# Kernel optimization log

Hardware: AMD Instinct MI355X
Metric: run time of the kernel (lower is better)

The kernel has to match this reference:

```python
import jax, jax.numpy as jnp
import numpy as np
from jax.scipy.special import gammaln, logsumexp

# Model dims (match init_kwargs)
N1, N2, N3 = 16, 16, 8          # n_state_list
S = N1 * N2 * N3                # tot_dim = 2048 flattened states
M = 16                          # m_dimensions
T = 16384                       # T_max


def setup_inputs() -> dict:
    key = jax.random.key(0)
    ks = jax.random.split(key, 10)
    # observed Poisson counts, shape (T, M)
    x = jax.random.randint(ks[0], (T, M), 0, 20)
    # per-factor Poisson rates: lambda_list[i] = exp(randn(N_i, M)) as in __init__
    lam1 = jnp.exp(jax.random.normal(ks[1], (N1, M), dtype=jnp.float32))
    lam2 = jnp.exp(jax.random.normal(ks[2], (N2, M), dtype=jnp.float32))
    lam3 = jnp.exp(jax.random.normal(ks[3], (N3, M), dtype=jnp.float32))
    # per-factor log transition matrices: softmax over dim 0 (A[next, prev] columns sum to 1)
    logA1 = jax.nn.log_softmax(jax.random.normal(ks[4], (N1, N1), dtype=jnp.float32), axis=0)
    logA2 = jax.nn.log_softmax(jax.random.normal(ks[5], (N2, N2), dtype=jnp.float32), axis=0)
    logA3 = jax.nn.log_softmax(jax.random.normal(ks[6], (N3, N3), dtype=jnp.float32), axis=0)
    # per-factor log state priors: log_softmax(rand(N)*10)
    logpi1 = jax.nn.log_softmax(jax.random.uniform(ks[7], (N1,), dtype=jnp.float32) * 10.0)
    logpi2 = jax.nn.log_softmax(jax.random.uniform(ks[8], (N2,), dtype=jnp.float32) * 10.0)
    logpi3 = jax.nn.log_softmax(jax.random.uniform(ks[9], (N3,), dtype=jnp.float32) * 10.0)
    return {"x": x, "lam1": lam1, "lam2": lam2, "lam3": lam3,
            "logA1": logA1, "logA2": logA2, "logA3": logA3,
            "logpi1": logpi1, "logpi2": logpi2, "logpi3": logpi3}


def reference(x, lam1, lam2, lam3, logA1, logA2, logA3, logpi1, logpi2, logpi3):
    # combine_lambdas: lam_c[s1,s2,s3,m] = lam1[s1,m] + lam2[s2,m] + lam3[s3,m]
    lam_c = (lam1[:, None, None, :] + lam2[None, :, None, :]
             + lam3[None, None, :, :]).reshape(S, M)  # (S, M)
    xf = x.astype(jnp.float32)
    # Poisson log-pmf summed over the M observation dims:
    # em[t, s] = sum_m x[t,m]*log(lam_c[s,m]) - lam_c[s,m] - lgamma(x[t,m]+1)
    em = (xf @ jnp.log(lam_c).T
          - lam_c.sum(axis=-1)[None, :]
          - gammaln(xf + 1.0).sum(axis=-1)[:, None])  # (T, S)
    # combined log transition: logA[dest_flat, prev_flat] = sum_i logA_i[d_i, p_i]
    logA = (logA1[:, None, None, :, None, None]
            + logA2[None, :, None, None, :, None]
            + logA3[None, None, :, None, None, :]).reshape(S, S)
    # combined log priors
    logpi = (logpi1[:, None, None] + logpi2[None, :, None]
             + logpi3[None, None, :]).reshape(S)
    # log-domain forward recurrence (log_alpha_calc)
    alpha0 = em[0] + logpi
    def step(prev, em_t):
        a = em_t + logsumexp(logA + prev[None, :], axis=1)
        return a, None
    alpha_last, _ = jax.lax.scan(step, alpha0, em[1:])
    # log p(x) = logsumexp over final-step alpha
    return logsumexp(alpha_last)
```

## Files before the change

### kernel.cpp

```cpp
#include <hip/hip_runtime.h>
#include <math.h>

#define TMAX 16384
#define MDIM 16
#define SD   2048
#define CLEN 16
#define WUP  16
#define CHKB 512
#define NS   (CLEN + WUP - 1)
#define EROWS 32

typedef unsigned int  uint;
typedef unsigned short ushort;
typedef __attribute__((ext_vector_type(8))) short short8;
typedef __attribute__((ext_vector_type(4))) short short4v;
typedef __attribute__((ext_vector_type(4))) float floatx4;
typedef __attribute__((ext_vector_type(2))) uint uintx2;

template<int CTRL>
__device__ __forceinline__ float fmax_dpp(float v) {
    int o = __builtin_amdgcn_update_dpp(__float_as_int(v), __float_as_int(v),
                                        CTRL, 0xf, 0xf, false);
    return fmaxf(v, __int_as_float(o));
}
__device__ __forceinline__ float waveMax64(float v) {
    v = fmax_dpp<0x111>(v);
    v = fmax_dpp<0x112>(v);
    v = fmax_dpp<0x114>(v);
    v = fmax_dpp<0x118>(v);
    v = fmax_dpp<0x142>(v);
    v = fmax_dpp<0x143>(v);
    return __int_as_float(__builtin_amdgcn_readlane(__float_as_int(v), 63));
}
__device__ __forceinline__ float waveSumF(float v) {
    #pragma unroll
    for (int o = 32; o > 0; o >>= 1) v += __shfl_xor(v, o, 64);
    return v;
}
__device__ __forceinline__ double waveSumD(double v) {
    #pragma unroll
    for (int o = 32; o > 0; o >>= 1) v += __shfl_xor(v, o, 64);
    return v;
}

__device__ __forceinline__ short f2bfs(float f) {
    uint u = __float_as_uint(f);
    return (short)((u + 0x7FFFu + ((u >> 16) & 1u)) >> 16);
}
__device__ __forceinline__ uint pkbf(float a, float b) {
    uint ua = __float_as_uint(a), ub = __float_as_uint(b);
    ua = (ua + 0x7FFFu + ((ua >> 16) & 1u)) >> 16;
    ub = (ub + 0x7FFFu + ((ub >> 16) & 1u)) & 0xFFFF0000u;
    return ua | ub;
}
__device__ __forceinline__ short4v pk4(float a, float b, float c, float d) {
    short4v r;
    r[0] = f2bfs(a); r[1] = f2bfs(b); r[2] = f2bfs(c); r[3] = f2bfs(d);
    return r;
}
__device__ __forceinline__ float bfl(uint u) { return __uint_as_float(u << 16); }
__device__ __forceinline__ float bfh(uint u) { return __uint_as_float(u & 0xFFFF0000u); }

#if __has_builtin(__builtin_amdgcn_mfma_f32_16x16x16bf16_1k)
#define MFMA16(a, b, c) __builtin_amdgcn_mfma_f32_16x16x16bf16_1k(a, b, c, 0, 0, 0)
#else
__device__ __forceinline__ floatx4 mfma16_asm(short4v a, short4v b, floatx4 c) {
    asm volatile("v_mfma_f32_16x16x16_bf16 %0, %1, %2, %0\n\t"
                 "s_nop 7\n\ts_nop 7"
                 : "+v"(c) : "v"(a), "v"(b));
    return c;
}
#define MFMA16(a, b, c) mfma16_asm(a, b, c)
#endif
#define MFMA32(a, b, c) __builtin_amdgcn_mfma_f32_16x16x32_bf16(a, b, c, 0, 0, 0)

__global__ __launch_bounds__(512, 2)
void emP_kernel(const int* __restrict__ x,
                const float* __restrict__ lam1,
                const float* __restrict__ lam2,
                const float* __restrict__ lam3,
                ushort* __restrict__ P,
                float* __restrict__ SumAuxArr,
                float* __restrict__ out) {
    __shared__ float wmx[EROWS][8];
    __shared__ float DemS[EROWS];
    __shared__ float lgtbl[32];
    __shared__ __align__(16) float xfs[EROWS * MDIM];
    __shared__ float lgred;
    const int tid = threadIdx.x, lane = tid & 63, wv = tid >> 6;
    const int q = lane >> 4, nn = lane & 15;
    const int d2 = 2 * wv + (nn >> 3);
    const int d3 = nn & 7;

    if (tid < 32) lgtbl[tid] = lgammaf((float)tid + 1.0f);
    if (tid == 0) lgred = 0.f;

    float llc[4][16], ls[4];
    #pragma unroll
    for (int j = 0; j < 4; ++j) {
        const int d1 = 4 * q + j;
        float sum = 0.f;
        #pragma unroll
        for (int m = 0; m < 16; ++m) {
            float la = lam1[d1 * 16 + m] + lam2[d2 * 16 + m] + lam3[d3 * 16 + m];
            sum += la;
            llc[j][m] = __logf(la);
        }
        ls[j] = sum;
    }

    const int t0 = blockIdx.x * EROWS;
    const int xv = x[t0 * MDIM + tid];
    xfs[tid] = (float)xv;
    __syncthreads();
    {
        double lg = (double)lgtbl[xv & 31];
        lg = waveSumD(lg);
        if (lane == 0) atomicAdd(&lgred, (float)lg);
    }

    float em[EROWS][4];
    #pragma unroll
    for (int ti = 0; ti < EROWS; ++ti) {
        float xr[16];
        *(float4*)&xr[0]  = *(const float4*)&xfs[ti * 16 + 0];
        *(float4*)&xr[4]  = *(const float4*)&xfs[ti * 16 + 4];
        *(float4*)&xr[8]  = *(const float4*)&xfs[ti * 16 + 8];
        *(float4*)&xr[12] = *(const float4*)&xfs[ti * 16 + 12];
        float vm = -3.4e38f;
        #pragma unroll
        for (int j = 0; j < 4; ++j) {
            float d = 0.f;
            #pragma unroll
            for (int m = 0; m < 16; ++m) d = fmaf(xr[m], llc[j][m], d);
            em[ti][j] = d - ls[j];
            vm = fmaxf(vm, em[ti][j]);
        }
        vm = waveMax64(vm);
        if (lane == 0) wmx[ti][wv] = vm;
    }
    __syncthreads();
    if (tid < 32) {
        float m = wmx[tid][0];
        #pragma unroll
        for (int i = 1; i < 8; ++i) m = fmaxf(m, wmx[tid][i]);
        DemS[tid] = m;
    }
    __syncthreads();

    #pragma unroll
    for (int ti = 0; ti < EROWS; ++ti) {
        const float Dem = DemS[ti];
        uint2 w;
        w.x = pkbf(__expf(em[ti][0] - Dem), __expf(em[ti][1] - Dem));
        w.y = pkbf(__expf(em[ti][2] - Dem), __expf(em[ti][3] - Dem));
        *(uint2*)(P + (size_t)(t0 + ti) * SD + tid * 4) = w;
    }

    if (tid == 0) {
        double sumD = 0.0;
        #pragma unroll
        for (int i = 0; i < EROWS; ++i) sumD += (double)DemS[i];
        SumAuxArr[blockIdx.x] = (float)sumD - lgred;
        if (blockIdx.x == 0) out[0] = 0.f;
    }
}

__global__ __launch_bounds__(512, 4)
void fhmm_chunk_kernel(const ushort* __restrict__ P,
                       const float* __restrict__ SumAuxArr,
                       const float* __restrict__ logA1,
                       const float* __restrict__ logA2,
                       const float* __restrict__ logA3,
                       const float* __restrict__ logpi1,
                       const float* __restrict__ logpi2,
                       const float* __restrict__ logpi3,
                       float* __restrict__ out)
{
    __shared__ __align__(16) short c1bA[2 * 2048];
    __shared__ __align__(16) short c1bB[2 * 2048];
    __shared__ float wmAA[8], wmAB[8];
    __shared__ float sred[8];
    __shared__ float saux8[8];

    const int tid  = threadIdx.x;
    const int lane = tid & 63;
    const int wv   = tid >> 6;
    const int q    = lane >> 4;
    const int ml   = lane & 15;

    const int b   = blockIdx.x;
    const int tA0 = (b == 0) ? 0 : 32 * b - 16;
    const int tB0 = 32 * b;

    short4v bA1k;
    #pragma unroll
    for (int j = 0; j < 4; ++j)
        bA1k[j] = f2bfs(__expf(logA1[ml * 16 + 4 * q + j]));

    const int d2p = 2 * wv + (ml >> 3);
    const int d3p = ml & 7;
    short8 bK[4];
    #pragma unroll
    for (int jc = 0; jc < 4; ++jc)
        #pragma unroll
        for (int i = 0; i < 8; ++i)
            bK[jc][i] = f2bfs(__expf(logA2[d2p * 16 + 4 * jc + q] + logA3[d3p * 8 + i]));

    const int oS1w = ml * 128 + ((((2 * wv + (q >> 1)) ^ ml) & 15) << 3) + 4 * (q & 1);
    int o23[4];
    #pragma unroll
    for (int jc = 0; jc < 4; ++jc)
        o23[jc] = ml * 128 + ((((4 * jc + q) ^ ml) & 15) << 3);

    if (b == 0) {
        float sx = waveSumF(SumAuxArr[tid]);
        if (lane == 0) saux8[wv] = sx;
    }

    double OFF = 0.0;
    float nuA[4], nuB[4];
    {
        uintx2 p0 = *(const uintx2*)(P + (size_t)tA0 * SD + tid * 4);
        if (b == 0) {
            float lp23 = logpi2[d2p] + logpi3[d3p];
            nuA[0] = bfl(p0.x) * __expf(logpi1[4 * q + 0] + lp23);
            nuA[1] = bfh(p0.x) * __expf(logpi1[4 * q + 1] + lp23);
            nuA[2] = bfl(p0.y) * __expf(logpi1[4 * q + 2] + lp23);
            nuA[3] = bfh(p0.y) * __expf(logpi1[4 * q + 3] + lp23);
        } else {
            nuA[0] = bfl(p0.x); nuA[1] = bfh(p0.x);
            nuA[2] = bfl(p0.y); nuA[3] = bfh(p0.y);
        }
    }
    {
        uintx2 p0 = *(const uintx2*)(P + (size_t)tB0 * SD + tid * 4);
        nuB[0] = bfl(p0.x); nuB[1] = bfh(p0.x);
        nuB[2] = bfl(p0.y); nuB[3] = bfh(p0.y);
    }

    uintx2 PbA0 = *(const uintx2*)(P + (size_t)(tA0 + 1) * SD + tid * 4);
    uintx2 PbA1 = *(const uintx2*)(P + (size_t)(tA0 + 2) * SD + tid * 4);
    uintx2 PbB0 = *(const uintx2*)(P + (size_t)(tB0 + 1) * SD + tid * 4);
    uintx2 PbB1 = *(const uintx2*)(P + (size_t)(tB0 + 2) * SD + tid * 4);

#define SSTEP(S, RESC, ACCFA, ACCFB)                                            \
{                                                                               \
    const int par = (S) & 1;          \
    short* cAq = c1bA + (par << 11);                                            \
    short* cBq = c1bB + (par << 11);                                            \
    {                                 \
        short4v afA = pk4(nuA[0], nuA[1], nuA[2], nuA[3]);                      \
        short4v afB = pk4(nuB[0], nuB[1], nuB[2], nuB[3]);                      \
        floatx4 sA = {0.f, 0.f, 0.f, 0.f};                                      \
        floatx4 sB = {0.f, 0.f, 0.f, 0.f};                                      \
        sA = MFMA16(afA, bA1k, sA);                                             \
        sB = MFMA16(afB, bA1k, sB);                                             \
        ((uintx2*)(cAq + oS1w))[0] = (uintx2){pkbf(sA[0], sA[1]), pkbf(sA[2], sA[3])}; \
        ((uintx2*)(cBq + oS1w))[0] = (uintx2){pkbf(sB[0], sB[1]), pkbf(sB[2], sB[3])}; \
    }                                                                           \
    __syncthreads();                                                            \
    const int tnA = (tA0 + (S) + 2 < TMAX) ? tA0 + (S) + 2 : TMAX - 1;          \
    const int tnB = (tB0 + (S) + 2 < TMAX) ? tB0 + (S) + 2 : TMAX - 1;          \
    uintx2 PbA2 = *(const uintx2*)(P + (size_t)tnA * SD + tid * 4);             \
    uintx2 PbB2 = *(const uintx2*)(P + (size_t)tnB * SD + tid * 4);             \
    float invA = 1.f, invB = 1.f;                                               \
    if (RESC) {                                                                 \
        float mpA = waveMax64(wmAA[lane & 7]);                                  \
        float mpB = waveMax64(wmAB[lane & 7]);                                  \
        float mgA = fmaxf(mpA, 1e-30f);                                         \
        float mgB = fmaxf(mpB, 1e-30f);                                         \
        invA = __builtin_amdgcn_rcpf(mgA);                                      \
        invB = __builtin_amdgcn_rcpf(mgB);                                      \
        if (tid == 0) {                                                         \
            if (ACCFA) OFF += (double)__logf(mgA);                              \
            if (ACCFB) OFF += (double)__logf(mgB);                              \
        }                                                                       \
    }                                                                           \
    {              \
        short8 fA0 = *(const short8*)(cAq + o23[0]);                            \
        short8 fA1 = *(const short8*)(cAq + o23[1]);                            \
        short8 fA2 = *(const short8*)(cAq + o23[2]);                            \
        short8 fA3 = *(const short8*)(cAq + o23[3]);                            \
        short8 fB0 = *(const short8*)(cBq + o23[0]);                            \
        short8 fB1 = *(const short8*)(cBq + o23[1]);                            \
        short8 fB2 = *(const short8*)(cBq + o23[2]);                            \
        short8 fB3 = *(const short8*)(cBq + o23[3]);                            \
        floatx4 aA0 = {0.f, 0.f, 0.f, 0.f};                                     \
        floatx4 aA1 = {0.f, 0.f, 0.f, 0.f};                                     \
        floatx4 aB0 = {0.f, 0.f, 0.f, 0.f};                                     \
        floatx4 aB1 = {0.f, 0.f, 0.f, 0.f};                                     \
        aA0 = MFMA32(fA0, bK[0], aA0);  aB0 = MFMA32(fB0, bK[0], aB0);          \
        aA1 = MFMA32(fA1, bK[1], aA1);  aB1 = MFMA32(fB1, bK[1], aB1);          \
        aA0 = MFMA32(fA2, bK[2], aA0);  aB0 = MFMA32(fB2, bK[2], aB0);          \
        aA1 = MFMA32(fA3, bK[3], aA1);  aB1 = MFMA32(fB3, bK[3], aB1);          \
        floatx4 accA = aA0 + aA1;                                               \
        floatx4 accB = aB0 + aB1;                                               \
        if (RESC) {                                                             \
            nuA[0] = bfl(PbA0.x) * accA[0] * invA;                              \
            nuA[1] = bfh(PbA0.x) * accA[1] * invA;                              \
            nuA[2] = bfl(PbA0.y) * accA[2] * invA;                              \
            nuA[3] = bfh(PbA0.y) * accA[3] * invA;                              \
            nuB[0] = bfl(PbB0.x) * accB[0] * invB;                              \
            nuB[1] = bfh(PbB0.x) * accB[1] * invB;                              \
            nuB[2] = bfl(PbB0.y) * accB[2] * invB;                              \
            nuB[3] = bfh(PbB0.y) * accB[3] * invB;                              \
        } else {                                                                \
            nuA[0] = bfl(PbA0.x) * accA[0];                                     \
            nuA[1] = bfh(PbA0.x) * accA[1];                                     \
            nuA[2] = bfl(PbA0.y) * accA[2];                                     \
            nuA[3] = bfh(PbA0.y) * accA[3];                                     \
            nuB[0] = bfl(PbB0.x) * accB[0];                                     \
            nuB[1] = bfh(PbB0.x) * accB[1];                                     \
            nuB[2] = bfl(PbB0.y) * accB[2];                                     \
            nuB[3] = bfh(PbB0.y) * accB[3];                                     \
            float waA = waveMax64(fmaxf(fmaxf(nuA[0], nuA[1]), fmaxf(nuA[2], nuA[3]))); \
            float waB = waveMax64(fmaxf(fmaxf(nuB[0], nuB[1]), fmaxf(nuB[2], nuB[3]))); \
            if (lane == 0) { wmAA[wv] = waA; wmAB[wv] = waB; }                  \
        }                                                                       \
    }                                                                           \
    PbA0 = PbA1; PbA1 = PbA2; PbB0 = PbB1; PbB1 = PbB2;                         \
}

    SSTEP(1, false, false, false);
    for (int s = 2; s < NS; s += 2) {
        const bool accfA = (b == 0) || (s > WUP);
        const bool accfB = (s > WUP);
        SSTEP(s, true, accfA, accfB);
        SSTEP(s + 1, false, false, false);
    }
#undef SSTEP

    __syncthreads();

    if (b == CHKB - 1) {
        float su = waveSumF(nuB[0] + nuB[1] + nuB[2] + nuB[3]);
        if (lane == 0) sred[wv] = su;
        __syncthreads();
        if (tid == 0) {
            float mpA = wmAA[0];
            #pragma unroll
            for (int i = 1; i < 8; ++i) mpA = fmaxf(mpA, wmAA[i]);
            OFF += (double)__logf(fmaxf(mpA, 1e-30f));
            float tot = 0.f;
            #pragma unroll
            for (int i = 0; i < 8; ++i) tot += sred[i];
            OFF += (double)__logf(tot);
            atomicAdd(out, (float)OFF);
        }
    } else {
        if (tid == 0) {
            float mpA = wmAA[0], mpB = wmAB[0];
            #pragma unroll
            for (int i = 1; i < 8; ++i) {
                mpA = fmaxf(mpA, wmAA[i]);
                mpB = fmaxf(mpB, wmAB[i]);
            }
            OFF += (double)__logf(fmaxf(mpA, 1e-30f));
            OFF += (double)__logf(fmaxf(mpB, 1e-30f));
            if (b == 0) {
                float sa = 0.f;
                #pragma unroll
                for (int i = 0; i < 8; ++i) sa += saux8[i];
                OFF += (double)sa;
            }
            atomicAdd(out, (float)OFF);
        }
    }
}

extern "C" void kernel_launch(void* const* d_in, const int* in_sizes, int n_in,
                              void* d_out, int out_size, void* d_ws, size_t ws_size,
                              hipStream_t stream) {
    const int*   x      = (const int*)  d_in[0];
    const float* lam1   = (const float*)d_in[1];
    const float* lam2   = (const float*)d_in[2];
    const float* lam3   = (const float*)d_in[3];
    const float* logA1  = (const float*)d_in[4];
    const float* logA2  = (const float*)d_in[5];
    const float* logA3  = (const float*)d_in[6];
    const float* logpi1 = (const float*)d_in[7];
    const float* logpi2 = (const float*)d_in[8];
    const float* logpi3 = (const float*)d_in[9];
    float* out = (float*)d_out;

    float*  SumAuxArr = (float*)d_ws;
    ushort* P         = (ushort*)((char*)d_ws + 4096);

    emP_kernel <<<dim3(TMAX / EROWS), dim3(512), 0, stream>>>(
        x, lam1, lam2, lam3, P, SumAuxArr, out);
    fhmm_chunk_kernel<<<dim3(CHKB), dim3(512), 0, stream>>>(
        P, SumAuxArr, logA1, logA2, logA3, logpi1, logpi2, logpi3, out);
}
```

Before: 156.2 us.

## Fuse emission computation into chunked forward kernel and shorten warmup

Removes the separate emission kernel and its global bf16 P buffer. Each chunk block now computes the scaled emission probabilities for its own 40 rows (warmup plus two chunks) straight into registers, and the per-row max offsets are summed locally. The warmup length drops from 16 to 8 steps, which cuts recurrence steps per block. Costs and risks: emission rows are recomputed for overlapping warmup windows, register pressure rises from holding 40 rows, a memset launch is added, and the shorter warmup may loosen the approximation of the chunked recurrence.

```diff
diff --git a/kernel.cpp b/kernel.cpp
--- a/kernel.cpp
+++ b/kernel.cpp
@@ -3,12 +3,12 @@
 
 #define TMAX 16384
 #define MDIM 16
-#define SD   2048
 #define CLEN 16
-#define WUP  16
+#define WUP  8
 #define CHKB 512
 #define NS   (CLEN + WUP - 1)
-#define EROWS 32
+#define NROWS (2 * CLEN + WUP)
+#define HROWS 20
 
 typedef unsigned int  uint;
 typedef unsigned short ushort;
@@ -74,101 +74,11 @@
 #endif
 #define MFMA32(a, b, c) __builtin_amdgcn_mfma_f32_16x16x32_bf16(a, b, c, 0, 0, 0)
 
-__global__ __launch_bounds__(512, 2)
-void emP_kernel(const int* __restrict__ x,
-                const float* __restrict__ lam1,
-                const float* __restrict__ lam2,
-                const float* __restrict__ lam3,
-                ushort* __restrict__ P,
-                float* __restrict__ SumAuxArr,
-                float* __restrict__ out) {
-    __shared__ float wmx[EROWS][8];
-    __shared__ float DemS[EROWS];
-    __shared__ float lgtbl[32];
-    __shared__ __align__(16) float xfs[EROWS * MDIM];
-    __shared__ float lgred;
-    const int tid = threadIdx.x, lane = tid & 63, wv = tid >> 6;
-    const int q = lane >> 4, nn = lane & 15;
-    const int d2 = 2 * wv + (nn >> 3);
-    const int d3 = nn & 7;
-
-    if (tid < 32) lgtbl[tid] = lgammaf((float)tid + 1.0f);
-    if (tid == 0) lgred = 0.f;
-
-    float llc[4][16], ls[4];
-    #pragma unroll
-    for (int j = 0; j < 4; ++j) {
-        const int d1 = 4 * q + j;
-        float sum = 0.f;
-        #pragma unroll
-        for (int m = 0; m < 16; ++m) {
-            float la = lam1[d1 * 16 + m] + lam2[d2 * 16 + m] + lam3[d3 * 16 + m];
-            sum += la;
-            llc[j][m] = __logf(la);
-        }
-        ls[j] = sum;
-    }
-
-    const int t0 = blockIdx.x * EROWS;
-    const int xv = x[t0 * MDIM + tid];
-    xfs[tid] = (float)xv;
-    __syncthreads();
-    {
-        double lg = (double)lgtbl[xv & 31];
-        lg = waveSumD(lg);
-        if (lane == 0) atomicAdd(&lgred, (float)lg);
-    }
-
-    float em[EROWS][4];
-    #pragma unroll
-    for (int ti = 0; ti < EROWS; ++ti) {
-        float xr[16];
-        *(float4*)&xr[0]  = *(const float4*)&xfs[ti * 16 + 0];
-        *(float4*)&xr[4]  = *(const float4*)&xfs[ti * 16 + 4];
-        *(float4*)&xr[8]  = *(const float4*)&xfs[ti * 16 + 8];
-        *(float4*)&xr[12] = *(const float4*)&xfs[ti * 16 + 12];
-        float vm = -3.4e38f;
-        #pragma unroll
-        for (int j = 0; j < 4; ++j) {
-            float d = 0.f;
-            #pragma unroll
-            for (int m = 0; m < 16; ++m) d = fmaf(xr[m], llc[j][m], d);
-            em[ti][j] = d - ls[j];
-            vm = fmaxf(vm, em[ti][j]);
-        }
-        vm = waveMax64(vm);
-        if (lane == 0) wmx[ti][wv] = vm;
-    }
-    __syncthreads();
-    if (tid < 32) {
-        float m = wmx[tid][0];
-        #pragma unroll
-        for (int i = 1; i < 8; ++i) m = fmaxf(m, wmx[tid][i]);
-        DemS[tid] = m;
-    }
-    __syncthreads();
-
-    #pragma unroll
-    for (int ti = 0; ti < EROWS; ++ti) {
-        const float Dem = DemS[ti];
-        uint2 w;
-        w.x = pkbf(__expf(em[ti][0] - Dem), __expf(em[ti][1] - Dem));
-        w.y = pkbf(__expf(em[ti][2] - Dem), __expf(em[ti][3] - Dem));
-        *(uint2*)(P + (size_t)(t0 + ti) * SD + tid * 4) = w;
-    }
-
-    if (tid == 0) {
-        double sumD = 0.0;
-        #pragma unroll
-        for (int i = 0; i < EROWS; ++i) sumD += (double)DemS[i];
-        SumAuxArr[blockIdx.x] = (float)sumD - lgred;
-        if (blockIdx.x == 0) out[0] = 0.f;
-    }
-}
-
 __global__ __launch_bounds__(512, 4)
-void fhmm_chunk_kernel(const ushort* __restrict__ P,
-                       const float* __restrict__ SumAuxArr,
+void fhmm_fused_kernel(const int* __restrict__ x,
+                       const float* __restrict__ lam1,
+                       const float* __restrict__ lam2,
+                       const float* __restrict__ lam3,
                        const float* __restrict__ logA1,
                        const float* __restrict__ logA2,
                        const float* __restrict__ logA3,
@@ -181,77 +91,145 @@
     __shared__ __align__(16) short c1bB[2 * 2048];
     __shared__ float wmAA[8], wmAB[8];
     __shared__ float sred[8];
-    __shared__ float saux8[8];
+    __shared__ float wmx[HROWS][8];
+    __shared__ float DemS[NROWS];
+    __shared__ float lgtbl[32];
+    __shared__ __align__(16) float xfs[NROWS * MDIM];
+    __shared__ float lgred;
 
     const int tid  = threadIdx.x;
     const int lane = tid & 63;
     const int wv   = tid >> 6;
     const int q    = lane >> 4;
     const int ml   = lane & 15;
-
-    const int b   = blockIdx.x;
-    const int tA0 = (b == 0) ? 0 : 32 * b - 16;
-    const int tB0 = 32 * b;
+    const int d2   = 2 * wv + (ml >> 3);
+    const int d3   = ml & 7;
+
+    const int b     = blockIdx.x;
+    const int rbase = 32 * b - WUP;
+
+    if (tid < 32) lgtbl[tid] = lgammaf((float)tid + 1.0f);
+    if (tid == 0) lgred = 0.f;
+
+    {
+        int g0 = rbase + (tid >> 4);
+        if (g0 < 0) g0 = 0;
+        xfs[tid] = (float)x[g0 * MDIM + (tid & 15)];
+        if (tid < NROWS * MDIM - 512) {
+            int i = tid + 512;
+            xfs[i] = (float)x[(rbase + (i >> 4)) * MDIM + (i & 15)];
+        }
+    }
+
+    float llc[4][16], ls[4];
+    #pragma unroll
+    for (int j = 0; j < 4; ++j) {
+        const int d1 = 4 * q + j;
+        float sum = 0.f;
+        #pragma unroll
+        for (int m = 0; m < 16; ++m) {
+            float la = lam1[d1 * 16 + m] + lam2[d2 * 16 + m] + lam3[d3 * 16 + m];
+            sum += la;
+            llc[j][m] = __logf(la);
+        }
+        ls[j] = sum;
+    }
+    __syncthreads();
+
+    {
+        int xv = x[32 * b * MDIM + tid];
+        double lg = (double)lgtbl[xv & 31];
+        lg = waveSumD(lg);
+        if (lane == 0) atomicAdd(&lgred, (float)lg);
+    }
+
+    uintx2 Pr[NROWS];
+    float em[HROWS][4];
+    #pragma unroll
+    for (int h = 0; h < 2; ++h) {
+        #pragma unroll
+        for (int r = 0; r < HROWS; ++r) {
+            const int k = HROWS * h + r;
+            float xr[16];
+            *(float4*)&xr[0]  = *(const float4*)&xfs[k * 16 + 0];
+            *(float4*)&xr[4]  = *(const float4*)&xfs[k * 16 + 4];
+            *(float4*)&xr[8]  = *(const float4*)&xfs[k * 16 + 8];
+            *(float4*)&xr[12] = *(const float4*)&xfs[k * 16 + 12];
+            float vm = -3.4e38f;
+            #pragma unroll
+            for (int j = 0; j < 4; ++j) {
+                float d = 0.f;
+                #pragma unroll
+                for (int m = 0; m < 16; ++m) d = fmaf(xr[m], llc[j][m], d);
+                em[r][j] = d - ls[j];
+                vm = fmaxf(vm, em[r][j]);
+            }
+            vm = waveMax64(vm);
+            if (lane == 0) wmx[r][wv] = vm;
+        }
+        __syncthreads();
+        if (tid < HROWS) {
+            float m = wmx[tid][0];
+            #pragma unroll
+            for (int i = 1; i < 8; ++i) m = fmaxf(m, wmx[tid][i]);
+            DemS[HROWS * h + tid] = m;
+        }
+        __syncthreads();
+        #pragma unroll
+        for (int r = 0; r < HROWS; ++r) {
+            const int k = HROWS * h + r;
+            const float Dem = DemS[k];
+            uintx2 w;
+            w.x = pkbf(__expf(em[r][0] - Dem), __expf(em[r][1] - Dem));
+            w.y = pkbf(__expf(em[r][2] - Dem), __expf(em[r][3] - Dem));
+            Pr[k] = w;
+        }
+    }
 
     short4v bA1k;
     #pragma unroll
     for (int j = 0; j < 4; ++j)
         bA1k[j] = f2bfs(__expf(logA1[ml * 16 + 4 * q + j]));
-
-    const int d2p = 2 * wv + (ml >> 3);
-    const int d3p = ml & 7;
     short8 bK[4];
     #pragma unroll
     for (int jc = 0; jc < 4; ++jc)
         #pragma unroll
         for (int i = 0; i < 8; ++i)
-            bK[jc][i] = f2bfs(__expf(logA2[d2p * 16 + 4 * jc + q] + logA3[d3p * 8 + i]));
-
+            bK[jc][i] = f2bfs(__expf(logA2[d2 * 16 + 4 * jc + q] + logA3[d3 * 8 + i]));
     const int oS1w = ml * 128 + ((((2 * wv + (q >> 1)) ^ ml) & 15) << 3) + 4 * (q & 1);
     int o23[4];
     #pragma unroll
     for (int jc = 0; jc < 4; ++jc)
         o23[jc] = ml * 128 + ((((4 * jc + q) ^ ml) & 15) << 3);
 
+    double OFF = 0.0;
+    float nuA0, nuA1, nuA2, nuA3, nuB0, nuB1, nuB2, nuB3;
     if (b == 0) {
-        float sx = waveSumF(SumAuxArr[tid]);
-        if (lane == 0) saux8[wv] = sx;
-    }
-
-    double OFF = 0.0;
-    float nuA[4], nuB[4];
+        uintx2 p0 = Pr[WUP];
+        float lp23 = logpi2[d2] + logpi3[d3];
+        nuA0 = bfl(p0.x) * __expf(logpi1[4 * q + 0] + lp23);
+        nuA1 = bfh(p0.x) * __expf(logpi1[4 * q + 1] + lp23);
+        nuA2 = bfl(p0.y) * __expf(logpi1[4 * q + 2] + lp23);
+        nuA3 = bfh(p0.y) * __expf(logpi1[4 * q + 3] + lp23);
+    } else {
+        uintx2 p0 = Pr[0];
+        nuA0 = bfl(p0.x); nuA1 = bfh(p0.x);
+        nuA2 = bfl(p0.y); nuA3 = bfh(p0.y);
+    }
     {
-        uintx2 p0 = *(const uintx2*)(P + (size_t)tA0 * SD + tid * 4);
-        if (b == 0) {
-            float lp23 = logpi2[d2p] + logpi3[d3p];
-            nuA[0] = bfl(p0.x) * __expf(logpi1[4 * q + 0] + lp23);
-            nuA[1] = bfh(p0.x) * __expf(logpi1[4 * q + 1] + lp23);
-            nuA[2] = bfl(p0.y) * __expf(logpi1[4 * q + 2] + lp23);
-            nuA[3] = bfh(p0.y) * __expf(logpi1[4 * q + 3] + lp23);
-        } else {
-            nuA[0] = bfl(p0.x); nuA[1] = bfh(p0.x);
-            nuA[2] = bfl(p0.y); nuA[3] = bfh(p0.y);
-        }
-    }
-    {
-        uintx2 p0 = *(const uintx2*)(P + (size_t)tB0 * SD + tid * 4);
-        nuB[0] = bfl(p0.x); nuB[1] = bfh(p0.x);
-        nuB[2] = bfl(p0.y); nuB[3] = bfh(p0.y);
-    }
-
-    uintx2 PbA0 = *(const uintx2*)(P + (size_t)(tA0 + 1) * SD + tid * 4);
-    uintx2 PbA1 = *(const uintx2*)(P + (size_t)(tA0 + 2) * SD + tid * 4);
-    uintx2 PbB0 = *(const uintx2*)(P + (size_t)(tB0 + 1) * SD + tid * 4);
-    uintx2 PbB1 = *(const uintx2*)(P + (size_t)(tB0 + 2) * SD + tid * 4);
-
-#define SSTEP(S, RESC, ACCFA, ACCFB)                                            \
+        uintx2 p0 = Pr[CLEN];
+        nuB0 = bfl(p0.x); nuB1 = bfh(p0.x);
+        nuB2 = bfl(p0.y); nuB3 = bfh(p0.y);
+    }
+
+#define SSTEP(S, RESC, KOFFA)                                                   \
 {                                                                               \
-    const int par = (S) & 1;          \
+    const int par = (S) & 1;                                                    \
     short* cAq = c1bA + (par << 11);                                            \
     short* cBq = c1bB + (par << 11);                                            \
-    {                                 \
-        short4v afA = pk4(nuA[0], nuA[1], nuA[2], nuA[3]);                      \
-        short4v afB = pk4(nuB[0], nuB[1], nuB[2], nuB[3]);                      \
+    {                                                 \
+        short4v afA = pk4(nuA0, nuA1, nuA2, nuA3);                              \
+        short4v afB = pk4(nuB0, nuB1, nuB2, nuB3);                              \
         floatx4 sA = {0.f, 0.f, 0.f, 0.f};                                      \
         floatx4 sB = {0.f, 0.f, 0.f, 0.f};                                      \
         sA = MFMA16(afA, bA1k, sA);                                             \
@@ -260,10 +238,6 @@
         ((uintx2*)(cBq + oS1w))[0] = (uintx2){pkbf(sB[0], sB[1]), pkbf(sB[2], sB[3])}; \
     }                                                                           \
     __syncthreads();                                                            \
-    const int tnA = (tA0 + (S) + 2 < TMAX) ? tA0 + (S) + 2 : TMAX - 1;          \
-    const int tnB = (tB0 + (S) + 2 < TMAX) ? tB0 + (S) + 2 : TMAX - 1;          \
-    uintx2 PbA2 = *(const uintx2*)(P + (size_t)tnA * SD + tid * 4);             \
-    uintx2 PbB2 = *(const uintx2*)(P + (size_t)tnB * SD + tid * 4);             \
     float invA = 1.f, invB = 1.f;                                               \
     if (RESC) {                                                                 \
         float mpA = waveMax64(wmAA[lane & 7]);                                  \
@@ -273,11 +247,11 @@
         invA = __builtin_amdgcn_rcpf(mgA);                                      \
         invB = __builtin_amdgcn_rcpf(mgB);                                      \
         if (tid == 0) {                                                         \
-            if (ACCFA) OFF += (double)__logf(mgA);                              \
-            if (ACCFB) OFF += (double)__logf(mgB);                              \
+            if ((KOFFA) == WUP || (S) > WUP) OFF += (double)__logf(mgA);        \
+            if ((S) > WUP)                   OFF += (double)__logf(mgB);        \
         }                                                                       \
     }                                                                           \
-    {              \
+    {                                               \
         short8 fA0 = *(const short8*)(cAq + o23[0]);                            \
         short8 fA1 = *(const short8*)(cAq + o23[1]);                            \
         short8 fA2 = *(const short8*)(cAq + o23[2]);                            \
@@ -296,45 +270,54 @@
         aA1 = MFMA32(fA3, bK[3], aA1);  aB1 = MFMA32(fB3, bK[3], aB1);          \
         floatx4 accA = aA0 + aA1;                                               \
         floatx4 accB = aB0 + aB1;                                               \
+        uintx2 PA = Pr[(S) + (KOFFA)];                                          \
+        uintx2 PB = Pr[(S) + CLEN];                                             \
         if (RESC) {                                                             \
-            nuA[0] = bfl(PbA0.x) * accA[0] * invA;                              \
-            nuA[1] = bfh(PbA0.x) * accA[1] * invA;                              \
-            nuA[2] = bfl(PbA0.y) * accA[2] * invA;                              \
-            nuA[3] = bfh(PbA0.y) * accA[3] * invA;                              \
-            nuB[0] = bfl(PbB0.x) * accB[0] * invB;                              \
-            nuB[1] = bfh(PbB0.x) * accB[1] * invB;                              \
-            nuB[2] = bfl(PbB0.y) * accB[2] * invB;                              \
-            nuB[3] = bfh(PbB0.y) * accB[3] * invB;                              \
+            nuA0 = bfl(PA.x) * accA[0] * invA;                                  \
+            nuA1 = bfh(PA.x) * accA[1] * invA;                                  \
+            nuA2 = bfl(PA.y) * accA[2] * invA;                                  \
+            nuA3 = bfh(PA.y) * accA[3] * invA;                                  \
+            nuB0 = bfl(PB.x) * accB[0] * invB;                                  \
+            nuB1 = bfh(PB.x) * accB[1] * invB;                                  \
+            nuB2 = bfl(PB.y) * accB[2] * invB;                                  \
+            nuB3 = bfh(PB.y) * accB[3] * invB;                                  \
         } else {                                                                \
-            nuA[0] = bfl(PbA0.x) * accA[0];                                     \
-            nuA[1] = bfh(PbA0.x) * accA[1];                                     \
-            nuA[2] = bfl(PbA0.y) * accA[2];                                     \
-            nuA[3] = bfh(PbA0.y) * accA[3];                                     \
-            nuB[0] = bfl(PbB0.x) * accB[0];                                     \
-            nuB[1] = bfh(PbB0.x) * accB[1];                                     \
-            nuB[2] = bfl(PbB0.y) * accB[2];                                     \
-            nuB[3] = bfh(PbB0.y) * accB[3];                                     \
-            float waA = waveMax64(fmaxf(fmaxf(nuA[0], nuA[1]), fmaxf(nuA[2], nuA[3]))); \
-            float waB = waveMax64(fmaxf(fmaxf(nuB[0], nuB[1]), fmaxf(nuB[2], nuB[3]))); \
+            nuA0 = bfl(PA.x) * accA[0];                                         \
+            nuA1 = bfh(PA.x) * accA[1];                                         \
+            nuA2 = bfl(PA.y) * accA[2];                                         \
+            nuA3 = bfh(PA.y) * accA[3];                                         \
+            nuB0 = bfl(PB.x) * accB[0];                                         \
+            nuB1 = bfh(PB.x) * accB[1];                                         \
+            nuB2 = bfl(PB.y) * accB[2];                                         \
+            nuB3 = bfh(PB.y) * accB[3];                                         \
+            float waA = waveMax64(fmaxf(fmaxf(nuA0, nuA1), fmaxf(nuA2, nuA3))); \
+            float waB = waveMax64(fmaxf(fmaxf(nuB0, nuB1), fmaxf(nuB2, nuB3))); \
             if (lane == 0) { wmAA[wv] = waA; wmAB[wv] = waB; }                  \
         }                                                                       \
     }                                                                           \
-    PbA0 = PbA1; PbA1 = PbA2; PbB0 = PbB1; PbB1 = PbB2;                         \
-}
-
-    SSTEP(1, false, false, false);
-    for (int s = 2; s < NS; s += 2) {
-        const bool accfA = (b == 0) || (s > WUP);
-        const bool accfB = (s > WUP);
-        SSTEP(s, true, accfA, accfB);
-        SSTEP(s + 1, false, false, false);
+}
+
+    if (b == 0) {
+        SSTEP(1, false, WUP);
+        #pragma unroll
+        for (int s2 = 2; s2 < NS; s2 += 2) {
+            SSTEP(s2, true, WUP);
+            SSTEP(s2 + 1, false, WUP);
+        }
+    } else {
+        SSTEP(1, false, 0);
+        #pragma unroll
+        for (int s2 = 2; s2 < NS; s2 += 2) {
+            SSTEP(s2, true, 0);
+            SSTEP(s2 + 1, false, 0);
+        }
     }
 #undef SSTEP
 
     __syncthreads();
 
     if (b == CHKB - 1) {
-        float su = waveSumF(nuB[0] + nuB[1] + nuB[2] + nuB[3]);
+        float su = waveSumF(nuB0 + nuB1 + nuB2 + nuB3);
         if (lane == 0) sred[wv] = su;
         __syncthreads();
         if (tid == 0) {
@@ -346,6 +329,10 @@
             #pragma unroll
             for (int i = 0; i < 8; ++i) tot += sred[i];
             OFF += (double)__logf(tot);
+            double sumD = 0.0;
+            #pragma unroll
+            for (int k = WUP; k < NROWS; ++k) sumD += (double)DemS[k];
+            OFF += sumD - (double)lgred;
             atomicAdd(out, (float)OFF);
         }
     } else {
@@ -358,12 +345,10 @@
             }
             OFF += (double)__logf(fmaxf(mpA, 1e-30f));
             OFF += (double)__logf(fmaxf(mpB, 1e-30f));
-            if (b == 0) {
-                float sa = 0.f;
-                #pragma unroll
-                for (int i = 0; i < 8; ++i) sa += saux8[i];
-                OFF += (double)sa;
-            }
+            double sumD = 0.0;
+            #pragma unroll
+            for (int k = WUP; k < NROWS; ++k) sumD += (double)DemS[k];
+            OFF += sumD - (double)lgred;
             atomicAdd(out, (float)OFF);
         }
     }
@@ -384,11 +369,7 @@
     const float* logpi3 = (const float*)d_in[9];
     float* out = (float*)d_out;
 
-    float*  SumAuxArr = (float*)d_ws;
-    ushort* P         = (ushort*)((char*)d_ws + 4096);
-
-    emP_kernel <<<dim3(TMAX / EROWS), dim3(512), 0, stream>>>(
-        x, lam1, lam2, lam3, P, SumAuxArr, out);
-    fhmm_chunk_kernel<<<dim3(CHKB), dim3(512), 0, stream>>>(
-        P, SumAuxArr, logA1, logA2, logA3, logpi1, logpi2, logpi3, out);
-}
+    hipMemsetAsync(out, 0, sizeof(float), stream);
+    fhmm_fused_kernel<<<dim3(CHKB), dim3(512), 0, stream>>>(
+        x, lam1, lam2, lam3, logA1, logA2, logA3, logpi1, logpi2, logpi3, out);
+}
```

Result: slower. 362.8 us (+132.2%).
